# Performance work log

Measured on AMD Instinct MI355X. Metric: run time of the kernel, lower is better.

## Reference

```python
import jax, jax.numpy as jnp
import numpy as np


def setup_inputs() -> dict:
    key = jax.random.key(0)
    k1, k2, k3 = jax.random.split(key, 3)
    b, c, h, w = 4, 64, 64, 64
    content = jax.random.normal(k1, (b, c, h, w), dtype=jnp.float32)
    content_s = jax.random.normal(k2, (b, c, h, w), dtype=jnp.float32)
    style = jax.random.normal(k3, (b, c, h, w), dtype=jnp.float32)
    return {"content": content, "content_s": content_s, "style": style}


def reference(content, content_s, style):
    b, c, h, w = content.shape
    hw = h * w
    Fc = content.reshape(b, c, hw)      # [b, c, HW]
    Fs = content_s.reshape(b, c, hw)    # [b, c, HW]
    Fst = style.reshape(b, c, hw)       # [b, c, HW]
    # S[b, q, k] = sum_c Fc[b, c, q] * Fs[b, c, k]  (Fc transposed as in torch)
    S = jnp.einsum('bcq,bck->bqk', Fc, Fs)
    S = jax.nn.softmax(S, axis=-1)
    # O = style @ S^T : O[b, c, q] = sum_k Fst[b, c, k] * S[b, q, k]
    O = jnp.einsum('bck,bqk->bcq', Fst, S).reshape(b, c, h, w)
    return jnp.concatenate((content, O), axis=1)
```

## Files before the change

### kernel.cpp

```cpp
#include <hip/hip_runtime.h>
#include <math.h>


#define Bb 4
#define Cc 64
#define HWs 4096
#define SPLITS 8
#define TPS 8
#define RLOG2E 1.44269504088896340736f

typedef _Float16 half8 __attribute__((ext_vector_type(8)));
typedef _Float16 half4 __attribute__((ext_vector_type(4)));
typedef float floatx4 __attribute__((ext_vector_type(4)));

__global__ __launch_bounds__(256) void prep_k(const float* __restrict__ content,
                                              const float* __restrict__ Fc,
                                              const float* __restrict__ Fs,
                                              const float* __restrict__ Fst,
                                              float* __restrict__ out,
                                              _Float16* __restrict__ Qt,
                                              _Float16* __restrict__ Kt,
                                              _Float16* __restrict__ Vt) {
    const int bid = blockIdx.x;
    const int t = threadIdx.x;
    const int sect = bid >> 10;
    if (sect == 0) {
        int i4 = bid * 256 + t;
        const float4* c4 = (const float4*)content;
        const float4* v4 = (const float4*)Fst;
        float4* o4 = (float4*)out;
        int b = i4 >> 16, rem = i4 & 65535;
        o4[(size_t)b * 131072 + rem] = c4[i4];
        float4 v = v4[i4];
        half4 h;
        h[0] = (_Float16)v.x; h[1] = (_Float16)v.y;
        h[2] = (_Float16)v.z; h[3] = (_Float16)v.w;
        *(half4*)(Vt + (size_t)i4 * 4) = h;
    } else {
        __shared__ _Float16 T[16][72];
        int e = bid & 1023;
        int b = e >> 8;
        int hw0 = (e & 255) * 16;
        const float* src = (sect == 1) ? Fs : Fc;
        _Float16* dst = (sect == 1) ? Kt : Qt;
        const float scale = (sect == 1) ? 1.0f : RLOG2E;
        const float* sb = src + (size_t)b * Cc * HWs;
        {
            int c = t >> 2, x4 = (t & 3) * 4;
            float4 v = *(const float4*)(sb + (size_t)c * HWs + hw0 + x4);
            T[x4 + 0][c] = (_Float16)(v.x * scale);
            T[x4 + 1][c] = (_Float16)(v.y * scale);
            T[x4 + 2][c] = (_Float16)(v.z * scale);
            T[x4 + 3][c] = (_Float16)(v.w * scale);
        }
        __syncthreads();
        if (t < 128) {
            int row = t >> 3, g = t & 7;
            _Float16* db = dst + (size_t)b * HWs * Cc;
            *(half8*)(db + (size_t)(hw0 + row) * Cc + g * 8) = *(half8*)&T[row][g * 8];
        }
    }
}

__global__ __launch_bounds__(256, 2) void attn_k(const _Float16* __restrict__ Qt,
                                                 const _Float16* __restrict__ Kt,
                                                 const _Float16* __restrict__ Vt,
                                                 _Float16* __restrict__ Opart,
                                                 float2* __restrict__ ml) {
    const int tid  = threadIdx.x;
    const int w    = tid >> 6;
    const int lane = tid & 63;
    const int quad = lane >> 4;
    const int l15  = lane & 15;
    const int qg = blockIdx.x & 15;
    const int b  = (blockIdx.x >> 4) & 3;
    const int s  = blockIdx.x >> 6;
    const int k0base = s * TPS * 64;
    const int qbase = qg * 256 + w * 64 + l15;

    __shared__ _Float16 Kl[2][64 * 64];
    __shared__ _Float16 Vl[2][64 * 64];
    __shared__ _Float16 Ps[4][2][16][72];

    const _Float16* Qb = Qt + (size_t)b * HWs * Cc;
    const _Float16* Kb = Kt + (size_t)b * HWs * Cc;
    const _Float16* Vb = Vt + (size_t)b * Cc * HWs;

    const bool isK  = tid < 128;
    const int  sl   = tid & 127;
    const int  srow = sl >> 3;
    const int  sjg  = sl & 7;
    const int  ssw  = (sjg ^ (srow & 7)) * 8;

    half8 qf[4][2];
    #pragma unroll
    for (int g = 0; g < 4; ++g) {
        qf[g][0] = *(const half8*)(Qb + (size_t)(qbase + g * 16) * Cc + quad * 8);
        qf[g][1] = *(const half8*)(Qb + (size_t)(qbase + g * 16) * Cc + 32 + quad * 8);
    }

    half8 st[4];
    auto stage_load = [&](int kt) {
        int kk0 = k0base + kt * 64;
        #pragma unroll
        for (int i = 0; i < 4; ++i) {
            int row = srow + 16 * i;
            if (isK) st[i] = *(const half8*)(Kb + (size_t)(kk0 + row) * 64 + sjg * 8);
            else     st[i] = *(const half8*)(Vb + (size_t)row * HWs + kk0 + sjg * 8);
        }
    };
    auto stage_write = [&](int p) {
        #pragma unroll
        for (int i = 0; i < 4; ++i) {
            int row = srow + 16 * i;
            if (isK) *(half8*)&Kl[p][row * 64 + ssw] = st[i];
            else     *(half8*)&Vl[p][row * 64 + ssw] = st[i];
        }
    };

    floatx4 acc[4][4];
    #pragma unroll
    for (int g = 0; g < 4; ++g)
        #pragma unroll
        for (int m = 0; m < 4; ++m) acc[g][m] = (floatx4)(0.0f);
    float m_run[4] = {-INFINITY, -INFINITY, -INFINITY, -INFINITY};
    float lsum[4] = {0.0f, 0.0f, 0.0f, 0.0f};

    stage_load(0);
    stage_write(0);
    stage_load(1);
    __syncthreads();

    const int swl = (l15 & 7);
    for (int kt = 0; kt < TPS; ++kt) {
        const int p = kt & 1;
        if (kt + 1 < TPS) stage_write(p ^ 1);
        if (kt + 2 < TPS) stage_load(kt + 2);

        floatx4 sv[4][4];
        #pragma unroll
        for (int m = 0; m < 4; ++m) {
            half8 ka0 = *(const half8*)&Kl[p][(m * 16 + l15) * 64 + ((quad ^ swl) * 8)];
            half8 ka1 = *(const half8*)&Kl[p][(m * 16 + l15) * 64 + (((4 + quad) ^ swl) * 8)];
            #pragma unroll
            for (int g = 0; g < 4; ++g) {
                sv[g][m] = __builtin_amdgcn_mfma_f32_16x16x32_f16(ka0, qf[g][0], (floatx4)(0.0f), 0, 0, 0);
                sv[g][m] = __builtin_amdgcn_mfma_f32_16x16x32_f16(ka1, qf[g][1], sv[g][m], 0, 0, 0);
            }
        }

        half8 va[4][2];
        #pragma unroll
        for (int m = 0; m < 4; ++m)
            #pragma unroll
            for (int ks = 0; ks < 2; ++ks)
                va[m][ks] = *(const half8*)&Vl[p][(m * 16 + l15) * 64 + (((ks * 4 + quad) ^ swl) * 8)];

        #pragma unroll
        for (int g = 0; g < 4; ++g) {
            float mx = -INFINITY;
            #pragma unroll
            for (int m = 0; m < 4; ++m)
                #pragma unroll
                for (int r = 0; r < 4; ++r) mx = fmaxf(mx, sv[g][m][r]);
            mx = fmaxf(mx, __shfl_xor(mx, 16));
            mx = fmaxf(mx, __shfl_xor(mx, 32));
            float m_new = fmaxf(m_run[g], mx);
            float alpha = exp2f(m_run[g] - m_new);
            m_run[g] = m_new;
            float part = 0.0f;
            #pragma unroll
            for (int m = 0; m < 4; ++m)
                #pragma unroll
                for (int r = 0; r < 4; ++r) {
                    float e = exp2f(sv[g][m][r] - m_new);
                    sv[g][m][r] = e;
                    part += e;
                }
            lsum[g] = lsum[g] * alpha + part;
            #pragma unroll
            for (int m = 0; m < 4; ++m)
                #pragma unroll
                for (int r = 0; r < 4; ++r) acc[g][m][r] *= alpha;

            #pragma unroll
            for (int m = 0; m < 4; ++m) {
                half4 pp;
                pp[0] = (_Float16)sv[g][m][0]; pp[1] = (_Float16)sv[g][m][1];
                pp[2] = (_Float16)sv[g][m][2]; pp[3] = (_Float16)sv[g][m][3];
                *(half4*)&Ps[w][g & 1][l15][m * 16 + quad * 4] = pp;
            }
            half8 pb0 = *(half8*)&Ps[w][g & 1][l15][quad * 8];
            half8 pb1 = *(half8*)&Ps[w][g & 1][l15][32 + quad * 8];

            #pragma unroll
            for (int m = 0; m < 4; ++m) {
                acc[g][m] = __builtin_amdgcn_mfma_f32_16x16x32_f16(va[m][0], pb0, acc[g][m], 0, 0, 0);
                acc[g][m] = __builtin_amdgcn_mfma_f32_16x16x32_f16(va[m][1], pb1, acc[g][m], 0, 0, 0);
            }
        }

        __syncthreads();
    }

    _Float16* op = Opart + (((size_t)s * Bb + b) * Cc) * HWs;
    #pragma unroll
    for (int g = 0; g < 4; ++g) {
        lsum[g] += __shfl_xor(lsum[g], 16);
        lsum[g] += __shfl_xor(lsum[g], 32);
        int q = qbase + g * 16;
        #pragma unroll
        for (int m = 0; m < 4; ++m)
            #pragma unroll
            for (int r = 0; r < 4; ++r) {
                int c = m * 16 + quad * 4 + r;
                op[(size_t)c * HWs + q] = (_Float16)acc[g][m][r];
            }
        if (quad == 0)
            ml[((size_t)b * HWs + q) * SPLITS + s] = make_float2(m_run[g], lsum[g]);
    }
}

__global__ __launch_bounds__(256) void combine_k(const _Float16* __restrict__ Opart,
                                                 const float2* __restrict__ ml,
                                                 float* __restrict__ out) {
    int idx = blockIdx.x * 256 + threadIdx.x;
    int q = idx & 4095;
    int c = (idx >> 12) & 63;
    int b = idx >> 18;
    const float2* mlp = ml + ((size_t)b * HWs + q) * SPLITS;
    float2 mls[SPLITS];
    #pragma unroll
    for (int s = 0; s < SPLITS; ++s) mls[s] = mlp[s];
    float M = -INFINITY;
    #pragma unroll
    for (int s = 0; s < SPLITS; ++s) M = fmaxf(M, mls[s].x);
    float l = 0.0f, wgt[SPLITS];
    #pragma unroll
    for (int s = 0; s < SPLITS; ++s) {
        wgt[s] = exp2f(mls[s].x - M);
        l += wgt[s] * mls[s].y;
    }
    float o = 0.0f;
    #pragma unroll
    for (int s = 0; s < SPLITS; ++s)
        o += wgt[s] * (float)Opart[(((size_t)s * Bb + b) * Cc + c) * HWs + q];
    out[((size_t)b * 2 * Cc + Cc + c) * HWs + q] = o / l;
}

extern "C" void kernel_launch(void* const* d_in, const int* in_sizes, int n_in,
                              void* d_out, int out_size, void* d_ws, size_t ws_size,
                              hipStream_t stream) {
    const float* content   = (const float*)d_in[0];
    const float* content_s = (const float*)d_in[1];
    const float* style     = (const float*)d_in[2];
    float* out = (float*)d_out;

    _Float16* Qt = (_Float16*)d_ws;
    _Float16* Kt = Qt + (size_t)Bb * HWs * Cc;
    _Float16* Vt = Kt + (size_t)Bb * HWs * Cc;
    _Float16* Opart = Vt + (size_t)Bb * Cc * HWs;
    float2*   ml = (float2*)(Opart + (size_t)SPLITS * Bb * Cc * HWs);

    prep_k<<<dim3(3072), dim3(256), 0, stream>>>(content, content, content_s, style,
                                                 out, Qt, Kt, Vt);
    attn_k<<<dim3(SPLITS * Bb * 16), dim3(256), 0, stream>>>(Qt, Kt, Vt, Opart, ml);
    combine_k<<<dim3(4096), dim3(256), 0, stream>>>(Opart, ml, out);
}
```

Before: 117.7 us.

## Load Q directly from fp32 content in attention and split score/softmax into halves

```diff
diff --git a/kernel.cpp b/kernel.cpp
--- a/kernel.cpp
+++ b/kernel.cpp
@@ -14,17 +14,14 @@
 typedef float floatx4 __attribute__((ext_vector_type(4)));
 
 __global__ __launch_bounds__(256) void prep_k(const float* __restrict__ content,
-                                              const float* __restrict__ Fc,
                                               const float* __restrict__ Fs,
                                               const float* __restrict__ Fst,
                                               float* __restrict__ out,
-                                              _Float16* __restrict__ Qt,
                                               _Float16* __restrict__ Kt,
                                               _Float16* __restrict__ Vt) {
     const int bid = blockIdx.x;
     const int t = threadIdx.x;
-    const int sect = bid >> 10;
-    if (sect == 0) {
+    if (bid < 1024) {
         int i4 = bid * 256 + t;
         const float4* c4 = (const float4*)content;
         const float4* v4 = (const float4*)Fst;
@@ -38,31 +35,28 @@
         *(half4*)(Vt + (size_t)i4 * 4) = h;
     } else {
         __shared__ _Float16 T[16][72];
-        int e = bid & 1023;
+        int e = bid - 1024;
         int b = e >> 8;
         int hw0 = (e & 255) * 16;
-        const float* src = (sect == 1) ? Fs : Fc;
-        _Float16* dst = (sect == 1) ? Kt : Qt;
-        const float scale = (sect == 1) ? 1.0f : RLOG2E;
-        const float* sb = src + (size_t)b * Cc * HWs;
+        const float* sb = Fs + (size_t)b * Cc * HWs;
         {
             int c = t >> 2, x4 = (t & 3) * 4;
             float4 v = *(const float4*)(sb + (size_t)c * HWs + hw0 + x4);
-            T[x4 + 0][c] = (_Float16)(v.x * scale);
-            T[x4 + 1][c] = (_Float16)(v.y * scale);
-            T[x4 + 2][c] = (_Float16)(v.z * scale);
-            T[x4 + 3][c] = (_Float16)(v.w * scale);
+            T[x4 + 0][c] = (_Float16)v.x;
+            T[x4 + 1][c] = (_Float16)v.y;
+            T[x4 + 2][c] = (_Float16)v.z;
+            T[x4 + 3][c] = (_Float16)v.w;
         }
         __syncthreads();
         if (t < 128) {
             int row = t >> 3, g = t & 7;
-            _Float16* db = dst + (size_t)b * HWs * Cc;
+            _Float16* db = Kt + (size_t)b * HWs * Cc;
             *(half8*)(db + (size_t)(hw0 + row) * Cc + g * 8) = *(half8*)&T[row][g * 8];
         }
     }
 }
 
-__global__ __launch_bounds__(256, 2) void attn_k(const _Float16* __restrict__ Qt,
+__global__ __launch_bounds__(256, 2) void attn_k(const float* __restrict__ Fc,
                                                  const _Float16* __restrict__ Kt,
                                                  const _Float16* __restrict__ Vt,
                                                  _Float16* __restrict__ Opart,
@@ -82,9 +76,9 @@
     __shared__ _Float16 Vl[2][64 * 64];
     __shared__ _Float16 Ps[4][2][16][72];
 
-    const _Float16* Qb = Qt + (size_t)b * HWs * Cc;
-    const _Float16* Kb = Kt + (size_t)b * HWs * Cc;
-    const _Float16* Vb = Vt + (size_t)b * Cc * HWs;
+    const float*    Fcb = Fc + (size_t)b * Cc * HWs;
+    const _Float16* Kb  = Kt + (size_t)b * HWs * Cc;
+    const _Float16* Vb  = Vt + (size_t)b * Cc * HWs;
 
     const bool isK  = tid < 128;
     const int  sl   = tid & 127;
@@ -94,10 +88,12 @@
 
     half8 qf[4][2];
     #pragma unroll
-    for (int g = 0; g < 4; ++g) {
-        qf[g][0] = *(const half8*)(Qb + (size_t)(qbase + g * 16) * Cc + quad * 8);
-        qf[g][1] = *(const half8*)(Qb + (size_t)(qbase + g * 16) * Cc + 32 + quad * 8);
-    }
+    for (int g = 0; g < 4; ++g)
+        #pragma unroll
+        for (int j = 0; j < 8; ++j) {
+            qf[g][0][j] = (_Float16)(Fcb[(size_t)(quad * 8 + j) * HWs + qbase + g * 16] * RLOG2E);
+            qf[g][1][j] = (_Float16)(Fcb[(size_t)(32 + quad * 8 + j) * HWs + qbase + g * 16] * RLOG2E);
+        }
 
     half8 st[4];
     auto stage_load = [&](int kt) {
@@ -137,18 +133,6 @@
         if (kt + 1 < TPS) stage_write(p ^ 1);
         if (kt + 2 < TPS) stage_load(kt + 2);
 
-        floatx4 sv[4][4];
-        #pragma unroll
-        for (int m = 0; m < 4; ++m) {
-            half8 ka0 = *(const half8*)&Kl[p][(m * 16 + l15) * 64 + ((quad ^ swl) * 8)];
-            half8 ka1 = *(const half8*)&Kl[p][(m * 16 + l15) * 64 + (((4 + quad) ^ swl) * 8)];
-            #pragma unroll
-            for (int g = 0; g < 4; ++g) {
-                sv[g][m] = __builtin_amdgcn_mfma_f32_16x16x32_f16(ka0, qf[g][0], (floatx4)(0.0f), 0, 0, 0);
-                sv[g][m] = __builtin_amdgcn_mfma_f32_16x16x32_f16(ka1, qf[g][1], sv[g][m], 0, 0, 0);
-            }
-        }
-
         half8 va[4][2];
         #pragma unroll
         for (int m = 0; m < 4; ++m)
@@ -157,46 +141,63 @@
                 va[m][ks] = *(const half8*)&Vl[p][(m * 16 + l15) * 64 + (((ks * 4 + quad) ^ swl) * 8)];
 
         #pragma unroll
-        for (int g = 0; g < 4; ++g) {
-            float mx = -INFINITY;
-            #pragma unroll
-            for (int m = 0; m < 4; ++m)
-                #pragma unroll
-                for (int r = 0; r < 4; ++r) mx = fmaxf(mx, sv[g][m][r]);
-            mx = fmaxf(mx, __shfl_xor(mx, 16));
-            mx = fmaxf(mx, __shfl_xor(mx, 32));
-            float m_new = fmaxf(m_run[g], mx);
-            float alpha = exp2f(m_run[g] - m_new);
-            m_run[g] = m_new;
-            float part = 0.0f;
-            #pragma unroll
-            for (int m = 0; m < 4; ++m)
-                #pragma unroll
-                for (int r = 0; r < 4; ++r) {
-                    float e = exp2f(sv[g][m][r] - m_new);
-                    sv[g][m][r] = e;
-                    part += e;
+        for (int h = 0; h < 2; ++h) {
+            floatx4 sv[2][4];
+            #pragma unroll
+            for (int m = 0; m < 4; ++m) {
+                half8 ka0 = *(const half8*)&Kl[p][(m * 16 + l15) * 64 + ((quad ^ swl) * 8)];
+                half8 ka1 = *(const half8*)&Kl[p][(m * 16 + l15) * 64 + (((4 + quad) ^ swl) * 8)];
+                #pragma unroll
+                for (int u = 0; u < 2; ++u) {
+                    const int g = h * 2 + u;
+                    sv[u][m] = __builtin_amdgcn_mfma_f32_16x16x32_f16(ka0, qf[g][0], (floatx4)(0.0f), 0, 0, 0);
+                    sv[u][m] = __builtin_amdgcn_mfma_f32_16x16x32_f16(ka1, qf[g][1], sv[u][m], 0, 0, 0);
                 }
-            lsum[g] = lsum[g] * alpha + part;
-            #pragma unroll
-            for (int m = 0; m < 4; ++m)
-                #pragma unroll
-                for (int r = 0; r < 4; ++r) acc[g][m][r] *= alpha;
-
-            #pragma unroll
-            for (int m = 0; m < 4; ++m) {
-                half4 pp;
-                pp[0] = (_Float16)sv[g][m][0]; pp[1] = (_Float16)sv[g][m][1];
-                pp[2] = (_Float16)sv[g][m][2]; pp[3] = (_Float16)sv[g][m][3];
-                *(half4*)&Ps[w][g & 1][l15][m * 16 + quad * 4] = pp;
             }
-            half8 pb0 = *(half8*)&Ps[w][g & 1][l15][quad * 8];
-            half8 pb1 = *(half8*)&Ps[w][g & 1][l15][32 + quad * 8];
-
-            #pragma unroll
-            for (int m = 0; m < 4; ++m) {
-                acc[g][m] = __builtin_amdgcn_mfma_f32_16x16x32_f16(va[m][0], pb0, acc[g][m], 0, 0, 0);
-                acc[g][m] = __builtin_amdgcn_mfma_f32_16x16x32_f16(va[m][1], pb1, acc[g][m], 0, 0, 0);
+
+            #pragma unroll
+            for (int u = 0; u < 2; ++u) {
+                const int g = h * 2 + u;
+                float mx = -INFINITY;
+                #pragma unroll
+                for (int m = 0; m < 4; ++m)
+                    #pragma unroll
+                    for (int r = 0; r < 4; ++r) mx = fmaxf(mx, sv[u][m][r]);
+                mx = fmaxf(mx, __shfl_xor(mx, 16));
+                mx = fmaxf(mx, __shfl_xor(mx, 32));
+                float m_new = fmaxf(m_run[g], mx);
+                float alpha = exp2f(m_run[g] - m_new);
+                m_run[g] = m_new;
+                float part = 0.0f;
+                #pragma unroll
+                for (int m = 0; m < 4; ++m)
+                    #pragma unroll
+                    for (int r = 0; r < 4; ++r) {
+                        float e = exp2f(sv[u][m][r] - m_new);
+                        sv[u][m][r] = e;
+                        part += e;
+                    }
+                lsum[g] = lsum[g] * alpha + part;
+                #pragma unroll
+                for (int m = 0; m < 4; ++m)
+                    #pragma unroll
+                    for (int r = 0; r < 4; ++r) acc[g][m][r] *= alpha;
+
+                #pragma unroll
+                for (int m = 0; m < 4; ++m) {
+                    half4 pp;
+                    pp[0] = (_Float16)sv[u][m][0]; pp[1] = (_Float16)sv[u][m][1];
+                    pp[2] = (_Float16)sv[u][m][2]; pp[3] = (_Float16)sv[u][m][3];
+                    *(half4*)&Ps[w][u][l15][m * 16 + quad * 4] = pp;
+                }
+                half8 pb0 = *(half8*)&Ps[w][u][l15][quad * 8];
+                half8 pb1 = *(half8*)&Ps[w][u][l15][32 + quad * 8];
+
+                #pragma unroll
+                for (int m = 0; m < 4; ++m) {
+                    acc[g][m] = __builtin_amdgcn_mfma_f32_16x16x32_f16(va[m][0], pb0, acc[g][m], 0, 0, 0);
+                    acc[g][m] = __builtin_amdgcn_mfma_f32_16x16x32_f16(va[m][1], pb1, acc[g][m], 0, 0, 0);
+                }
             }
         }
 
@@ -256,14 +257,12 @@
     const float* style     = (const float*)d_in[2];
     float* out = (float*)d_out;
 
-    _Float16* Qt = (_Float16*)d_ws;
-    _Float16* Kt = Qt + (size_t)Bb * HWs * Cc;
+    _Float16* Kt = (_Float16*)d_ws;
     _Float16* Vt = Kt + (size_t)Bb * HWs * Cc;
     _Float16* Opart = Vt + (size_t)Bb * Cc * HWs;
     float2*   ml = (float2*)(Opart + (size_t)SPLITS * Bb * Cc * HWs);
 
-    prep_k<<<dim3(3072), dim3(256), 0, stream>>>(content, content, content_s, style,
-                                                 out, Qt, Kt, Vt);
-    attn_k<<<dim3(SPLITS * Bb * 16), dim3(256), 0, stream>>>(Qt, Kt, Vt, Opart, ml);
+    prep_k<<<dim3(2048), dim3(256), 0, stream>>>(content, content_s, style, out, Kt, Vt);
+    attn_k<<<dim3(SPLITS * Bb * 16), dim3(256), 0, stream>>>(content, Kt, Vt, Opart, ml);
     combine_k<<<dim3(4096), dim3(256), 0, stream>>>(Opart, ml, out);
 }
```

After: 114.0 us. -3.1%, faster.
